# Kernel tuning notes

Measured on AMD Instinct MI355X. Metric: run time of the kernel, lower is better.

## Reference

```python
import jax, jax.numpy as jnp
import numpy as np

EPS = 1e-5


def clin(xr, xi, Wr, Wi, br, bi):
    # complex linear layer: (xr + i xi) @ (Wr + i Wi) + (br + i bi)
    yr = xr @ Wr - xi @ Wi + br
    yi = xr @ Wi + xi @ Wr + bi
    return yr, yi


def setup_inputs() -> dict:
    key = jax.random.key(0)
    ks = jax.random.split(key, 16)
    B, N, DE, DV = 4, 256, 128, 64
    s_in = 1.0 / np.sqrt(DE)
    s_p = 1.0 / np.sqrt(DV)
    f32 = jnp.float32
    inp = {
        'Z_q': jax.random.normal(ks[0], (B, 2, N, DE), f32),
        'Z_k': jax.random.normal(ks[1], (B, 2, N, DE), f32),
        'Z_v': jax.random.normal(ks[2], (B, 2, N, DE), f32),
        't_measure_all': jnp.tile(jnp.arange(N + 1, dtype=f32) * 0.01, (B, 1)),
        'Wq_r': jax.random.normal(ks[3], (DE, DV), f32) * s_in,
        'Wq_i': jax.random.normal(ks[4], (DE, DV), f32) * s_in,
        'bq_r': jnp.zeros((DV,), f32), 'bq_i': jnp.zeros((DV,), f32),
        'Wk_r': jax.random.normal(ks[5], (DE, DV), f32) * s_in,
        'Wk_i': jax.random.normal(ks[6], (DE, DV), f32) * s_in,
        'bk_r': jnp.zeros((DV,), f32), 'bk_i': jnp.zeros((DV,), f32),
        'Wv_r': jax.random.normal(ks[7], (DE, DV), f32) * s_in,
        'Wv_i': jax.random.normal(ks[8], (DE, DV), f32) * s_in,
        'bv_r': jnp.zeros((DV,), f32), 'bv_i': jnp.zeros((DV,), f32),
        'Wp_r': jax.random.normal(ks[9], (DV, DE), f32) * s_p,
        'Wp_i': jax.random.normal(ks[10], (DV, DE), f32) * s_p,
        'bp_r': jnp.zeros((DE,), f32), 'bp_i': jnp.zeros((DE,), f32),
        'lambda1': jax.random.normal(ks[11], (2, DV // 2), f32),
        'lambda_Omega_sqrt': jax.random.normal(ks[12], (DV,), f32) / DV,
        'lambda_Gamma_sqrt': jax.random.normal(ks[13], (DV,), f32) / DV,
        'noise_floor': jnp.array(1.0, f32),
        'tau': jnp.array(1.0, f32),
        'nu': jnp.array(1.0, f32),
        'eta_param': jnp.zeros((DV,), f32),
    }
    return inp


def reference(Z_q, Z_k, Z_v, t_measure_all,
              Wq_r, Wq_i, bq_r, bq_i, Wk_r, Wk_i, bk_r, bk_i,
              Wv_r, Wv_i, bv_r, bv_i, Wp_r, Wp_i, bp_r, bp_i,
              lambda1, lambda_Omega_sqrt, lambda_Gamma_sqrt,
              noise_floor, tau, nu, eta_param):
    N = Z_q.shape[2]
    # complex projections (B, N, d)
    Qr, Qi = clin(Z_q[:, 0], Z_q[:, 1], Wq_r, Wq_i, bq_r, bq_i)
    Kr_, Ki_ = clin(Z_k[:, 0], Z_k[:, 1], Wk_r, Wk_i, bk_r, bk_i)
    Vr, Vi = clin(Z_v[:, 0], Z_v[:, 1], Wv_r, Wv_i, bv_r, bv_i)
    # state-transition eigenvalues: stable conjugate pairs
    re = jnp.concatenate([-lambda1[0] ** 2, -lambda1[0] ** 2])  # (d_v,), Re<=0
    im = jnp.concatenate([lambda1[1], -lambda1[1]])             # (d_v,)
    lam_Om = lambda_Omega_sqrt ** 2
    lam_Ga = lambda_Gamma_sqrt ** 2 + EPS
    # pairwise complex exponential kernel exp(lambda * (t_i - t_j))
    t = t_measure_all[0, :-1]                       # (N,)
    dt = t[:, None] - t[None, :]                    # (N, N)
    amp = jnp.exp(re[None, None, :] * dt[:, :, None])
    ph = im[None, None, :] * dt[:, :, None]
    Ker = amp * jnp.cos(ph)                          # (N, N, d_v)
    Kei = amp * jnp.sin(ph)
    # propagated value estimates Z_hat_ij = exp(lam dt_ij) * V_j
    Zhr = Ker[None] * Vr[:, None] - Kei[None] * Vi[:, None]  # (B, N, N, d_v)
    Zhi = Ker[None] * Vi[:, None] + Kei[None] * Vr[:, None]
    # residuals R_ij = Q_i - exp(lam dt_ij) * K_j
    Rr = Qr[:, :, None, :] - (Ker[None] * Kr_[:, None] - Kei[None] * Ki_[:, None])
    Ri = Qi[:, :, None, :] - (Ker[None] * Ki_[:, None] + Kei[None] * Kr_[:, None])
    # per-pair covariance (OU-process propagation of measurement + process noise)
    adt = jnp.abs(dt)[:, :, None]
    exp2 = jnp.exp(2.0 * re * adt)                   # (N, N, d_v)
    Vij = lam_Ga * exp2 + lam_Om * (exp2 - 1.0) / (2.0 * (re - EPS))
    # mahalanobis distance and attention scores
    mah = (Rr ** 2 + Ri ** 2) / (Vij[None] + lam_Ga)          # (B, N, N, d_v)
    dist_sum = jnp.abs(nu) * jnp.sum(mah, axis=3, keepdims=True)
    base = Vij[None] * (noise_floor + dist_sum + EPS)
    scores = -jnp.abs(tau) * jnp.log(base)
    mask = jnp.tril(jnp.ones((N, N), bool))
    scores = jnp.where(mask[None, :, :, None], scores, -jnp.inf)
    Qij = jax.nn.softmax(scores, axis=2)             # normalize over j
    m = mask[None, :, :, None].astype(Zhr.dtype)
    Zhr = Zhr * m
    Zhi = Zhi * m
    est_vr = jnp.einsum('bijd,bijd->bid', Qij, Zhr)
    est_vi = jnp.einsum('bijd,bijd->bid', Qij, Zhi)
    # gated residual mix (double sigmoid as in source)
    eta = jax.nn.sigmoid(eta_param)
    g = jax.nn.sigmoid(eta)
    elr = (1.0 - eta) * Vr + g * est_vr
    eli = (1.0 - eta) * Vi + g * est_vi
    # one-step-ahead prediction via matrix exponential exp(lambda * h)
    h = t[1] - t[0]
    ma = jnp.exp(re * h)
    mr, mi = ma * jnp.cos(im * h), ma * jnp.sin(im * h)
    ppr = mr * elr - mi * eli
    ppi = mr * eli + mi * elr
    outr, outi = clin(ppr, ppi, Wp_r, Wp_i, bp_r, bp_i)
    est_latent = jnp.stack([elr, eli], axis=1)       # (B, 2, N, d_v)
    out = jnp.stack([outr, outi], axis=1)            # (B, 2, N, d_e)
    Zhat = jnp.stack([Zhr, Zhi], axis=1)             # (B, 2, N, N, d_v)
    lambda_h = jnp.stack([re, im])                   # (2, d_v)
    return est_latent, out, Qij, Zhat, lambda_h
```

## Files before the change

### kernel.cpp

```cpp
#include <hip/hip_runtime.h>
#include <math.h>

#define B_ 4
#define N_ 256
#define DE_ 128
#define DV_ 64
#define EPS_ 1e-5f

typedef __attribute__((ext_vector_type(4))) float f32x4;

__device__ __forceinline__ f32x4 ld4(const float* p) { return *(const f32x4*)p; }
__device__ __forceinline__ void st4(float* p, f32x4 v) { *(f32x4*)p = v; }
__device__ __forceinline__ void nt4(float* p, f32x4 v) { __builtin_nontemporal_store(v, (f32x4*)p); }

#define OFF_ETA   0
#define OFF_G     64
#define OFF_MR    128
#define OFF_MI    192
#define OFF_KER   256
#define OFF_KEI   (OFF_KER + N_*DV_)
#define OFF_A     (OFF_KEI + N_*DV_)
#define OFF_INV   (OFF_A + N_*DV_)
#define OFF_QR    (OFF_INV + N_*DV_)
#define OFF_QI    (OFF_QR + B_*N_*DV_)
#define OFF_KR    (OFF_QI + B_*N_*DV_)
#define OFF_KI    (OFF_KR + B_*N_*DV_)
#define OFF_VR    (OFF_KI + B_*N_*DV_)
#define OFF_VI    (OFF_VR + B_*N_*DV_)

#define OUT_EL    0
#define OUT_OUT   (B_*2*N_*DV_)
#define OUT_QIJ   (OUT_OUT + B_*2*N_*DE_)
#define OUT_ZHAT  (OUT_QIJ + B_*N_*N_*DV_)
#define OUT_LAMH  (OUT_ZHAT + (size_t)B_*2*N_*N_*DV_)

__global__ __launch_bounds__(256) void k_pre(
    const float* __restrict__ Zq, const float* __restrict__ Zk, const float* __restrict__ Zv,
    const float* __restrict__ Wqr, const float* __restrict__ Wqi,
    const float* __restrict__ bqr, const float* __restrict__ bqi,
    const float* __restrict__ Wkr, const float* __restrict__ Wki,
    const float* __restrict__ bkr, const float* __restrict__ bki,
    const float* __restrict__ Wvr, const float* __restrict__ Wvi,
    const float* __restrict__ bvr, const float* __restrict__ bvi,
    const float* __restrict__ t,  const float* __restrict__ lam1,
    const float* __restrict__ lOm, const float* __restrict__ lGa,
    const float* __restrict__ eta_p, const float* __restrict__ tau_p,
    float* __restrict__ ws, float* __restrict__ out)
{
    const int tid = (int)threadIdx.x;
    const int wv = tid >> 6;
    const int d = tid & 63;

    if (blockIdx.x >= 256) {
        const int idx = (int)blockIdx.x - 256;
        const int delta = idx * 4 + wv;

        const float l0 = lam1[d & 31];
        const float re = -l0 * l0;
        const float im = (d < 32) ? lam1[32 + d] : -lam1[d];

        const float lo = lOm[d];
        const float lam_Om = lo * lo;
        const float lg_ = lGa[d];
        const float lam_Ga = lg_ * lg_ + EPS_;
        const float tau_a = fabsf(tau_p[0]);

        const float t0 = t[0];
        const float dt = t[delta] - t0;

        const float amp = expf(re * dt);
        const float ph  = im * dt;
        const int td = delta * DV_ + d;
        ws[OFF_KER + td] = amp * cosf(ph);
        ws[OFF_KEI + td] = amp * sinf(ph);

        const float e2  = expf(2.0f * re * dt);
        const float vij = lam_Ga * e2 + lam_Om * (e2 - 1.0f) / (2.0f * (re - EPS_));
        ws[OFF_A   + td] = expf(-tau_a * logf(vij));
        ws[OFF_INV + td] = 1.0f / (vij + lam_Ga);

        if (delta == 0) {
            const float eta = 1.0f / (1.0f + expf(-eta_p[d]));
            const float g   = 1.0f / (1.0f + expf(-eta));
            ws[OFF_ETA + d] = eta;
            ws[OFF_G   + d] = g;
            const float h  = t[1] - t0;
            const float ma = expf(re * h);
            ws[OFF_MR + d] = ma * cosf(im * h);
            ws[OFF_MI + d] = ma * sinf(im * h);
            out[OUT_LAMH + d]       = re;
            out[OUT_LAMH + DV_ + d] = im;
        }
        return;
    }

    const int row0 = (int)blockIdx.x * 4;
    const int b = row0 >> 8;
    const int n0 = row0 & (N_ - 1);

    __shared__ float x[4][6][DE_];
    #pragma unroll
    for (int it = 0; it < 3; ++it) {
        const int v = tid + it * 256;
        const int seg = v >> 5;
        const int pos = v & 31;
        const int r = seg & 3;
        const int a = seg >> 2;
        const int m = a >> 1;
        const int c = a & 1;
        const float* src = (m == 0) ? Zq : ((m == 1) ? Zk : Zv);
        const f32x4 val = ld4(src + ((size_t)(b*2 + c)*N_ + (n0 + r))*DE_ + pos*4);
        st4(&x[r][a][pos*4], val);
    }
    __syncthreads();

    const int row = row0 + wv;
    float aqr = 0.f, aqi = 0.f, akr = 0.f, aki = 0.f, avr = 0.f, avi = 0.f;
    #pragma unroll 8
    for (int k = 0; k < DE_; ++k) {
        const float xqr = x[wv][0][k], xqi = x[wv][1][k];
        const float xkr = x[wv][2][k], xki = x[wv][3][k];
        const float xvr = x[wv][4][k], xvi = x[wv][5][k];
        float wr, wi;
        wr = Wqr[k*DV_ + d]; wi = Wqi[k*DV_ + d];
        aqr += xqr*wr - xqi*wi; aqi += xqr*wi + xqi*wr;
        wr = Wkr[k*DV_ + d]; wi = Wki[k*DV_ + d];
        akr += xkr*wr - xki*wi; aki += xkr*wi + xki*wr;
        wr = Wvr[k*DV_ + d]; wi = Wvi[k*DV_ + d];
        avr += xvr*wr - xvi*wi; avi += xvr*wi + xvi*wr;
    }
    const int o = row * DV_ + d;
    ws[OFF_QR + o] = aqr + bqr[d];
    ws[OFF_QI + o] = aqi + bqi[d];
    ws[OFF_KR + o] = akr + bkr[d];
    ws[OFF_KI + o] = aki + bki[d];
    ws[OFF_VR + o] = avr + bvr[d];
    ws[OFF_VI + o] = avi + bvi[d];
}

__global__ __launch_bounds__(256) void k_main2(
    const float* __restrict__ ws, float* __restrict__ out,
    const float* __restrict__ Wpr, const float* __restrict__ Wpi,
    const float* __restrict__ bpr, const float* __restrict__ bpi,
    const float* __restrict__ nf_p, const float* __restrict__ tau_p,
    const float* __restrict__ nu_p)
{
    const int vb = (int)blockIdx.x;
    const int b = vb & 3;
    const int i = (N_ - 1) - (vb >> 2);
    const int row = b * N_ + i;
    const int tid = (int)threadIdx.x;
    const int wv = tid >> 6;
    const int l = tid & 63;
    const int g = l >> 4;
    const int q16 = l & 15;
    const int dq = q16 * 4;

    __shared__ float wl[N_];
    __shared__ f32x4 redS[4][16];
    __shared__ f32x4 redR[4][16];
    __shared__ f32x4 redI[4][16];
    __shared__ float ppr_s[DV_], ppi_s[DV_];

    const float nf    = nf_p[0];
    const float tau_a = fabsf(tau_p[0]);
    const float nu_a  = fabsf(nu_p[0]);

    const f32x4 qr4 = ld4(ws + OFF_QR + row*DV_ + dq);
    const f32x4 qi4 = ld4(ws + OFF_QI + row*DV_ + dq);

    const int nfull = (i + 1) >> 2;
    const int tail  = (i + 1) & 3;
    const f32x4 z4 = {0.f,0.f,0.f,0.f};

    float* qij = out + OUT_QIJ + (size_t)row * N_ * DV_;
    float* zro = out + OUT_ZHAT + ((size_t)(b*2+0)*N_ + i) * N_ * DV_;
    float* zio = out + OUT_ZHAT + ((size_t)(b*2+1)*N_ + i) * N_ * DV_;

    f32x4 s4  = {0.f,0.f,0.f,0.f};
    f32x4 evr = {0.f,0.f,0.f,0.f};
    f32x4 evi = {0.f,0.f,0.f,0.f};
    #pragma unroll 2
    for (int T = wv; T < nfull; T += 4) {
        const int j = 4*T + g;
        const int o = j*DV_ + dq;
        const int td = (i - j)*DV_ + dq;
        const f32x4 ker = ld4(ws + OFF_KER + td);
        const f32x4 kei = ld4(ws + OFF_KEI + td);
        const f32x4 vnv = ld4(ws + OFF_INV + td);
        const f32x4 a4  = ld4(ws + OFF_A   + td);
        const int kj = (b*N_ + j)*DV_ + dq;
        const f32x4 kr = ld4(ws + OFF_KR + kj);
        const f32x4 ki = ld4(ws + OFF_KI + kj);
        const f32x4 vr = ld4(ws + OFF_VR + kj);
        const f32x4 vi = ld4(ws + OFF_VI + kj);
        const f32x4 rr = qr4 - (ker*kr - kei*ki);
        const f32x4 ri = qi4 - (ker*ki + kei*kr);
        const f32x4 mah = (rr*rr + ri*ri) * vnv;
        float ds = mah[0] + mah[1] + mah[2] + mah[3];
        ds += __shfl_xor(ds, 1);
        ds += __shfl_xor(ds, 2);
        ds += __shfl_xor(ds, 4);
        ds += __shfl_xor(ds, 8);
        const float wj = expf(-tau_a * logf(nf + nu_a*ds + EPS_));
        if (q16 == 0) wl[j] = wj;
        const f32x4 zr = ker*vr - kei*vi;
        const f32x4 zi = ker*vi + kei*vr;
        nt4(zro + o, zr);
        nt4(zio + o, zi);
        const f32x4 qn = a4 * wj;
        s4  += qn;
        evr += qn * zr;
        evi += qn * zi;
    }
    if (tail && ((nfull & 3) == wv)) {
        const int j = 4*nfull + g;
        const int o = j*DV_ + dq;
        const bool act = (g < tail);
        const int td = (act ? (i - j) : 0)*DV_ + dq;
        const f32x4 ker = ld4(ws + OFF_KER + td);
        const f32x4 kei = ld4(ws + OFF_KEI + td);
        const f32x4 vnv = ld4(ws + OFF_INV + td);
        const f32x4 a4  = ld4(ws + OFF_A   + td);
        const int kj = (b*N_ + (act ? j : 0))*DV_ + dq;
        const f32x4 kr = ld4(ws + OFF_KR + kj);
        const f32x4 ki = ld4(ws + OFF_KI + kj);
        const f32x4 vr = ld4(ws + OFF_VR + kj);
        const f32x4 vi = ld4(ws + OFF_VI + kj);
        const f32x4 rr = qr4 - (ker*kr - kei*ki);
        const f32x4 ri = qi4 - (ker*ki + kei*kr);
        const f32x4 mah = (rr*rr + ri*ri) * vnv;
        float ds = mah[0] + mah[1] + mah[2] + mah[3];
        ds += __shfl_xor(ds, 1);
        ds += __shfl_xor(ds, 2);
        ds += __shfl_xor(ds, 4);
        ds += __shfl_xor(ds, 8);
        if (act) {
            const float wj = expf(-tau_a * logf(nf + nu_a*ds + EPS_));
            if (q16 == 0) wl[j] = wj;
            const f32x4 zr = ker*vr - kei*vi;
            const f32x4 zi = ker*vi + kei*vr;
            nt4(zro + o, zr);
            nt4(zio + o, zi);
            const f32x4 qn = a4 * wj;
            s4  += qn;
            evr += qn * zr;
            evi += qn * zi;
        } else {
            nt4(zro + o, z4);
            nt4(zio + o, z4);
        }
    }
    {
        const int jz0 = 4 * (nfull + (tail ? 1 : 0));
        const int nq = (N_ - jz0) * 16;
        for (int u = tid; u < nq; u += 256) {
            const int o = jz0*DV_ + u*4;
            nt4(zro + o, z4);
            nt4(zio + o, z4);
        }
    }

    #pragma unroll
    for (int mask = 16; mask <= 32; mask <<= 1) {
        #pragma unroll
        for (int c = 0; c < 4; ++c) {
            s4[c]  += __shfl_xor(s4[c],  mask);
            evr[c] += __shfl_xor(evr[c], mask);
            evi[c] += __shfl_xor(evi[c], mask);
        }
    }
    if (g == 0) { redS[wv][q16] = s4; redR[wv][q16] = evr; redI[wv][q16] = evi; }
    __syncthreads();
    const f32x4 Z = redS[0][q16] + redS[1][q16] + redS[2][q16] + redS[3][q16];
    const f32x4 one = {1.f,1.f,1.f,1.f};
    const f32x4 invZ = one / Z;

    #pragma unroll 2
    for (int T = wv; T < nfull; T += 4) {
        const int j = 4*T + g;
        const int o = j*DV_ + dq;
        const int td = (i - j)*DV_ + dq;
        const f32x4 q4 = ld4(ws + OFF_A + td) * wl[j] * invZ;
        nt4(qij + o, q4);
    }
    if (tail && ((nfull & 3) == wv)) {
        const int j = 4*nfull + g;
        const int o = j*DV_ + dq;
        if (g < tail) {
            const int td = (i - j)*DV_ + dq;
            const f32x4 q4 = ld4(ws + OFF_A + td) * wl[j] * invZ;
            nt4(qij + o, q4);
        } else {
            nt4(qij + o, z4);
        }
    }
    {
        const int jz0 = 4 * (nfull + (tail ? 1 : 0));
        const int nq = (N_ - jz0) * 16;
        for (int u = tid; u < nq; u += 256) {
            nt4(qij + jz0*DV_ + u*4, z4);
        }
    }

    if (tid < 16) {
        const f32x4 Zt = redS[0][tid] + redS[1][tid] + redS[2][tid] + redS[3][tid];
        const f32x4 iZ = one / Zt;
        const f32x4 Evr = (redR[0][tid] + redR[1][tid] + redR[2][tid] + redR[3][tid]) * iZ;
        const f32x4 Evi = (redI[0][tid] + redI[1][tid] + redI[2][tid] + redI[3][tid]) * iZ;
        const int dq2 = tid * 4;
        const f32x4 vr  = ld4(ws + OFF_VR + row*DV_ + dq2);
        const f32x4 vi  = ld4(ws + OFF_VI + row*DV_ + dq2);
        const f32x4 eta = ld4(ws + OFF_ETA + dq2);
        const f32x4 gg  = ld4(ws + OFF_G + dq2);
        const f32x4 elr = (1.0f - eta)*vr + gg*Evr;
        const f32x4 eli = (1.0f - eta)*vi + gg*Evi;
        st4(out + OUT_EL + ((size_t)(b*2+0)*N_ + i)*DV_ + dq2, elr);
        st4(out + OUT_EL + ((size_t)(b*2+1)*N_ + i)*DV_ + dq2, eli);
        const f32x4 mr = ld4(ws + OFF_MR + dq2);
        const f32x4 mi = ld4(ws + OFF_MI + dq2);
        st4(ppr_s + dq2, mr*elr - mi*eli);
        st4(ppi_s + dq2, mr*eli + mi*elr);
    }
    __syncthreads();

    if (tid < DE_) {
        const int e = tid;
        float ar = bpr[e], ai = bpi[e];
        #pragma unroll 8
        for (int dd = 0; dd < DV_; ++dd) {
            const float wr = Wpr[dd*DE_ + e], wi = Wpi[dd*DE_ + e];
            const float r = ppr_s[dd], im = ppi_s[dd];
            ar += r*wr - im*wi;
            ai += r*wi + im*wr;
        }
        out[OUT_OUT + ((size_t)(b*2+0)*N_ + i)*DE_ + e] = ar;
        out[OUT_OUT + ((size_t)(b*2+1)*N_ + i)*DE_ + e] = ai;
    }
}

extern "C" void kernel_launch(void* const* d_in, const int* in_sizes, int n_in,
                              void* d_out, int out_size, void* d_ws, size_t ws_size,
                              hipStream_t stream)
{
    const float* Zq   = (const float*)d_in[0];
    const float* Zk   = (const float*)d_in[1];
    const float* Zv   = (const float*)d_in[2];
    const float* t    = (const float*)d_in[3];
    const float* Wqr  = (const float*)d_in[4];
    const float* Wqi  = (const float*)d_in[5];
    const float* bqr  = (const float*)d_in[6];
    const float* bqi  = (const float*)d_in[7];
    const float* Wkr  = (const float*)d_in[8];
    const float* Wki  = (const float*)d_in[9];
    const float* bkr  = (const float*)d_in[10];
    const float* bki  = (const float*)d_in[11];
    const float* Wvr  = (const float*)d_in[12];
    const float* Wvi  = (const float*)d_in[13];
    const float* bvr  = (const float*)d_in[14];
    const float* bvi  = (const float*)d_in[15];
    const float* Wpr  = (const float*)d_in[16];
    const float* Wpi  = (const float*)d_in[17];
    const float* bpr  = (const float*)d_in[18];
    const float* bpi  = (const float*)d_in[19];
    const float* lam1 = (const float*)d_in[20];
    const float* lOm  = (const float*)d_in[21];
    const float* lGa  = (const float*)d_in[22];
    const float* nf   = (const float*)d_in[23];
    const float* tau  = (const float*)d_in[24];
    const float* nu   = (const float*)d_in[25];
    const float* etap = (const float*)d_in[26];

    float* ws  = (float*)d_ws;
    float* out = (float*)d_out;

    k_pre<<<256 + 64, 256, 0, stream>>>(Zq, Zk, Zv,
                                        Wqr, Wqi, bqr, bqi,
                                        Wkr, Wki, bkr, bki,
                                        Wvr, Wvi, bvr, bvi,
                                        t, lam1, lOm, lGa, etap, tau, ws, out);
    k_main2<<<B_*N_, 256, 0, stream>>>(ws, out, Wpr, Wpi, bpr, bpi, nf, tau, nu);
}
```

Measured before the change: 68.25 us.

## Split projection over K across waves and use regular stores for big outputs

```diff
diff --git a/kernel.cpp b/kernel.cpp
--- a/kernel.cpp
+++ b/kernel.cpp
@@ -11,7 +11,6 @@
 
 __device__ __forceinline__ f32x4 ld4(const float* p) { return *(const f32x4*)p; }
 __device__ __forceinline__ void st4(float* p, f32x4 v) { *(f32x4*)p = v; }
-__device__ __forceinline__ void nt4(float* p, f32x4 v) { __builtin_nontemporal_store(v, (f32x4*)p); }
 
 #define OFF_ETA   0
 #define OFF_G     64
@@ -48,12 +47,12 @@
     float* __restrict__ ws, float* __restrict__ out)
 {
     const int tid = (int)threadIdx.x;
-    const int wv = tid >> 6;
-    const int d = tid & 63;
-
-    if (blockIdx.x >= 256) {
-        const int idx = (int)blockIdx.x - 256;
-        const int delta = idx * 4 + wv;
+
+    if (blockIdx.x >= 1024) {
+        const int idx = (int)blockIdx.x - 1024;
+        const int w = tid >> 6;
+        const int d = tid & 63;
+        const int delta = idx * 4 + w;
 
         const float l0 = lam1[d & 31];
         const float re = -l0 * l0;
@@ -94,33 +93,32 @@
         return;
     }
 
-    const int row0 = (int)blockIdx.x * 4;
-    const int b = row0 >> 8;
-    const int n0 = row0 & (N_ - 1);
-
-    __shared__ float x[4][6][DE_];
-    #pragma unroll
-    for (int it = 0; it < 3; ++it) {
-        const int v = tid + it * 256;
-        const int seg = v >> 5;
-        const int pos = v & 31;
-        const int r = seg & 3;
-        const int a = seg >> 2;
-        const int m = a >> 1;
-        const int c = a & 1;
-        const float* src = (m == 0) ? Zq : ((m == 1) ? Zk : Zv);
-        const f32x4 val = ld4(src + ((size_t)(b*2 + c)*N_ + (n0 + r))*DE_ + pos*4);
-        st4(&x[r][a][pos*4], val);
+    const int row = (int)blockIdx.x;
+    const int b = row >> 8, n = row & (N_ - 1);
+
+    __shared__ float x[6][DE_];
+    __shared__ float red[4][6][DV_];
+
+    if (tid < DE_) {
+        x[0][tid] = Zq[((size_t)(b*2+0)*N_ + n)*DE_ + tid];
+        x[1][tid] = Zq[((size_t)(b*2+1)*N_ + n)*DE_ + tid];
+        x[2][tid] = Zk[((size_t)(b*2+0)*N_ + n)*DE_ + tid];
+        x[3][tid] = Zk[((size_t)(b*2+1)*N_ + n)*DE_ + tid];
+        x[4][tid] = Zv[((size_t)(b*2+0)*N_ + n)*DE_ + tid];
+        x[5][tid] = Zv[((size_t)(b*2+1)*N_ + n)*DE_ + tid];
     }
     __syncthreads();
 
-    const int row = row0 + wv;
+    const int w = tid >> 6;
+    const int d = tid & 63;
     float aqr = 0.f, aqi = 0.f, akr = 0.f, aki = 0.f, avr = 0.f, avi = 0.f;
-    #pragma unroll 8
-    for (int k = 0; k < DE_; ++k) {
-        const float xqr = x[wv][0][k], xqi = x[wv][1][k];
-        const float xkr = x[wv][2][k], xki = x[wv][3][k];
-        const float xvr = x[wv][4][k], xvi = x[wv][5][k];
+    const int k0 = w * 32;
+    #pragma unroll 4
+    for (int kk = 0; kk < 32; ++kk) {
+        const int k = k0 + kk;
+        const float xqr = x[0][k], xqi = x[1][k];
+        const float xkr = x[2][k], xki = x[3][k];
+        const float xvr = x[4][k], xvi = x[5][k];
         float wr, wi;
         wr = Wqr[k*DV_ + d]; wi = Wqi[k*DV_ + d];
         aqr += xqr*wr - xqi*wi; aqi += xqr*wi + xqi*wr;
@@ -129,13 +127,20 @@
         wr = Wvr[k*DV_ + d]; wi = Wvi[k*DV_ + d];
         avr += xvr*wr - xvi*wi; avi += xvr*wi + xvi*wr;
     }
-    const int o = row * DV_ + d;
-    ws[OFF_QR + o] = aqr + bqr[d];
-    ws[OFF_QI + o] = aqi + bqi[d];
-    ws[OFF_KR + o] = akr + bkr[d];
-    ws[OFF_KI + o] = aki + bki[d];
-    ws[OFF_VR + o] = avr + bvr[d];
-    ws[OFF_VI + o] = avi + bvi[d];
+    red[w][0][d] = aqr; red[w][1][d] = aqi;
+    red[w][2][d] = akr; red[w][3][d] = aki;
+    red[w][4][d] = avr; red[w][5][d] = avi;
+    __syncthreads();
+
+    if (tid < DV_) {
+        const int o = row * DV_ + tid;
+        ws[OFF_QR + o] = red[0][0][tid]+red[1][0][tid]+red[2][0][tid]+red[3][0][tid] + bqr[tid];
+        ws[OFF_QI + o] = red[0][1][tid]+red[1][1][tid]+red[2][1][tid]+red[3][1][tid] + bqi[tid];
+        ws[OFF_KR + o] = red[0][2][tid]+red[1][2][tid]+red[2][2][tid]+red[3][2][tid] + bkr[tid];
+        ws[OFF_KI + o] = red[0][3][tid]+red[1][3][tid]+red[2][3][tid]+red[3][3][tid] + bki[tid];
+        ws[OFF_VR + o] = red[0][4][tid]+red[1][4][tid]+red[2][4][tid]+red[3][4][tid] + bvr[tid];
+        ws[OFF_VI + o] = red[0][5][tid]+red[1][5][tid]+red[2][5][tid]+red[3][5][tid] + bvi[tid];
+    }
 }
 
 __global__ __launch_bounds__(256) void k_main2(
@@ -206,8 +211,8 @@
         if (q16 == 0) wl[j] = wj;
         const f32x4 zr = ker*vr - kei*vi;
         const f32x4 zi = ker*vi + kei*vr;
-        nt4(zro + o, zr);
-        nt4(zio + o, zi);
+        st4(zro + o, zr);
+        st4(zio + o, zi);
         const f32x4 qn = a4 * wj;
         s4  += qn;
         evr += qn * zr;
@@ -240,15 +245,15 @@
             if (q16 == 0) wl[j] = wj;
             const f32x4 zr = ker*vr - kei*vi;
             const f32x4 zi = ker*vi + kei*vr;
-            nt4(zro + o, zr);
-            nt4(zio + o, zi);
+            st4(zro + o, zr);
+            st4(zio + o, zi);
             const f32x4 qn = a4 * wj;
             s4  += qn;
             evr += qn * zr;
             evi += qn * zi;
         } else {
-            nt4(zro + o, z4);
-            nt4(zio + o, z4);
+            st4(zro + o, z4);
+            st4(zio + o, z4);
         }
     }
     {
@@ -256,8 +261,8 @@
         const int nq = (N_ - jz0) * 16;
         for (int u = tid; u < nq; u += 256) {
             const int o = jz0*DV_ + u*4;
-            nt4(zro + o, z4);
-            nt4(zio + o, z4);
+            st4(zro + o, z4);
+            st4(zio + o, z4);
         }
     }
 
@@ -282,7 +287,7 @@
         const int o = j*DV_ + dq;
         const int td = (i - j)*DV_ + dq;
         const f32x4 q4 = ld4(ws + OFF_A + td) * wl[j] * invZ;
-        nt4(qij + o, q4);
+        st4(qij + o, q4);
     }
     if (tail && ((nfull & 3) == wv)) {
         const int j = 4*nfull + g;
@@ -290,16 +295,16 @@
         if (g < tail) {
             const int td = (i - j)*DV_ + dq;
             const f32x4 q4 = ld4(ws + OFF_A + td) * wl[j] * invZ;
-            nt4(qij + o, q4);
+            st4(qij + o, q4);
         } else {
-            nt4(qij + o, z4);
+            st4(qij + o, z4);
         }
     }
     {
         const int jz0 = 4 * (nfull + (tail ? 1 : 0));
         const int nq = (N_ - jz0) * 16;
         for (int u = tid; u < nq; u += 256) {
-            nt4(qij + jz0*DV_ + u*4, z4);
+            st4(qij + jz0*DV_ + u*4, z4);
         }
     }
 
@@ -374,10 +379,10 @@
     float* ws  = (float*)d_ws;
     float* out = (float*)d_out;
 
-    k_pre<<<256 + 64, 256, 0, stream>>>(Zq, Zk, Zv,
-                                        Wqr, Wqi, bqr, bqi,
-                                        Wkr, Wki, bkr, bki,
-                                        Wvr, Wvi, bvr, bvi,
-                                        t, lam1, lOm, lGa, etap, tau, ws, out);
+    k_pre<<<1024 + 64, 256, 0, stream>>>(Zq, Zk, Zv,
+                                         Wqr, Wqi, bqr, bqi,
+                                         Wkr, Wki, bkr, bki,
+                                         Wvr, Wvi, bvr, bvi,
+                                         t, lam1, lOm, lGa, etap, tau, ws, out);
     k_main2<<<B_*N_, 256, 0, stream>>>(ws, out, Wpr, Wpi, bpr, bpi, nf, tau, nu);
 }
```

After: 64.72 us. 1.05x faster.
